# Optimization experiments

Hardware: AMD Instinct MI355X
Metric: run time of the kernel (lower is better)

## Reference

```python
import jax, jax.numpy as jnp
import numpy as np

N = 50000   # num_nodes
D = 128     # h_dim
R = 32      # num_rels * 2 (forward + inverse relations)
B = 8       # num_bases
E = 600000  # num_edges


def setup_inputs() -> dict:
    key = jax.random.key(0)
    ks = jax.random.split(key, 14)
    s = 1.0 / np.sqrt(D)
    return {
        "h_ids": jnp.arange(N, dtype=jnp.int32),
        "src": jax.random.randint(ks[0], (E,), 0, N),
        "dst": jax.random.randint(ks[1], (E,), 0, N),
        "etype": jax.random.randint(ks[2], (E,), 0, R),
        "norm": jax.random.uniform(ks[3], (E, 1), dtype=jnp.float32),
        "embedding": jax.random.normal(ks[4], (N, D), dtype=jnp.float32) * 0.05,
        "w_comp1": jax.random.normal(ks[5], (R, B), dtype=jnp.float32) * (1.0 / np.sqrt(B)),
        "bases1": jax.random.normal(ks[6], (B, D, D), dtype=jnp.float32) * s,
        "loop_w1": jax.random.normal(ks[7], (D, D), dtype=jnp.float32) * s,
        "bias1": jnp.zeros((D,), dtype=jnp.float32),
        "w_comp2": jax.random.normal(ks[8], (R, B), dtype=jnp.float32) * (1.0 / np.sqrt(B)),
        "bases2": jax.random.normal(ks[9], (B, D, D), dtype=jnp.float32) * s,
        "loop_w2": jax.random.normal(ks[10], (D, D), dtype=jnp.float32) * s,
        "bias2": jnp.zeros((D,), dtype=jnp.float32),
    }


def _rel_graph_conv(h, src, dst, etype, norm, w_comp, bases, loop_w, bias, act):
    # basis decomposition: W[r] = sum_b w_comp[r,b] * bases[b]
    W = jnp.einsum('rb,bio->rio', w_comp, bases)          # [R, D, D]
    # transform every node by every relation weight (dense GEMM)
    all_t = jnp.einsum('ni,rio->nro', h, W)               # [N, R, D]
    # per-edge gather of relation-specific transformed source features
    msg = all_t[src, etype] * norm                        # [E, D]
    # scatter-aggregate messages at destination nodes
    agg = jax.ops.segment_sum(msg, dst, num_segments=h.shape[0])  # [N, D]
    out = agg + h @ loop_w + bias                         # self-loop + bias
    return act(out) if act is not None else out


def reference(h_ids, src, dst, etype, norm, embedding,
              w_comp1, bases1, loop_w1, bias1,
              w_comp2, bases2, loop_w2, bias2):
    # EmbeddingLayer
    h = embedding[h_ids]                                  # [N, D]
    # hidden layer 0: relu activation (idx < num_hidden_layers-1)
    h = _rel_graph_conv(h, src, dst, etype, norm, w_comp1, bases1, loop_w1, bias1, jax.nn.relu)
    # hidden layer 1: no activation (last layer)
    h = _rel_graph_conv(h, src, dst, etype, norm, w_comp2, bases2, loop_w2, bias2, None)
    return h
```

## Files before the change

### kernel.cpp

```cpp
#include <hip/hip_runtime.h>

#define DD 128
#define NB 8
#define KTOT 1152

typedef unsigned int uint_t;
typedef __attribute__((ext_vector_type(8))) _Float16 half8v;
typedef __attribute__((ext_vector_type(2))) _Float16 half2v;
typedef __attribute__((ext_vector_type(4))) float f32x4;

static __device__ __forceinline__ void gld_lds16(const _Float16* g, _Float16* l)
{
  __builtin_amdgcn_global_load_lds(
      (const __attribute__((address_space(1))) void*)g,
      (__attribute__((address_space(3))) void*)l, 16, 0, 0);
}

static __device__ __forceinline__ half2v bc_h2(uint_t u)
{
  union { uint_t u; half2v h; } c; c.u = u; return c.h;
}

static __device__ __forceinline__ float fdot2(uint_t a, uint_t b, float acc)
{
#if __has_builtin(__builtin_amdgcn_fdot2)
  return __builtin_amdgcn_fdot2(bc_h2(a), bc_h2(b), acc, false);
#else
  half2v x = bc_h2(a), y = bc_h2(b);
  return acc + (float)x[0] * (float)y[0] + (float)x[1] * (float)y[1];
#endif
}

__global__ __launch_bounds__(256) void k_prep_w(
    const float* __restrict__ bases1, const float* __restrict__ loopw1,
    const float* __restrict__ bases2, const float* __restrict__ loopw2,
    _Float16* __restrict__ WcA)
{
  int i = blockIdx.x * 256 + threadIdx.x;
  if (i >= 2 * 36 * DD * 32) return;
  int layer = i / (36 * DD * 32);
  int rem   = i % (36 * DD * 32);
  int ks    = rem / (DD * 32);
  int rem2  = rem % (DD * 32);
  int feat  = rem2 / 32;
  int j     = rem2 % 32;
  int k     = ks * 32 + j;
  const float* basesL = layer ? bases2 : bases1;
  const float* loopwL = layer ? loopw2 : loopw1;
  float v;
  if (k < 1024) {
    int kk = k >> 3, b = k & 7;
    v = basesL[((size_t)b * DD + kk) * DD + feat];
  } else {
    v = loopwL[(size_t)(k - 1024) * DD + feat];
  }
  WcA[i] = (_Float16)v;
}

__global__ __launch_bounds__(256) void k_cast(
    const float* __restrict__ h, const int* __restrict__ ids,
    _Float16* __restrict__ hf, int N)
{
  int i = blockIdx.x * 256 + threadIdx.x;
  if (i >= N * (DD / 8)) return;
  int n  = i / (DD / 8);
  int k8 = (i % (DD / 8)) * 8;
  int row = ids ? ids[n] : n;
  const float* hp = h + (size_t)row * DD + k8;
  float4 v0 = *(const float4*)hp;
  float4 v1 = *(const float4*)(hp + 4);
  union { _Float16 e[8]; uint4 q; } p;
  p.e[0]=(_Float16)v0.x; p.e[1]=(_Float16)v0.y; p.e[2]=(_Float16)v0.z; p.e[3]=(_Float16)v0.w;
  p.e[4]=(_Float16)v1.x; p.e[5]=(_Float16)v1.y; p.e[6]=(_Float16)v1.z; p.e[7]=(_Float16)v1.w;
  *(uint4*)&hf[(size_t)n * DD + k8] = p.q;
}

__global__ __launch_bounds__(256) void k_zero(int* __restrict__ p, int n)
{
  int i = blockIdx.x * 256 + threadIdx.x;
  if (i < n) p[i] = 0;
}

__global__ __launch_bounds__(256) void k_hist(
    const int* __restrict__ dst, int* __restrict__ cnt, int E)
{
  int e = blockIdx.x * 256 + threadIdx.x;
  if (e < E) atomicAdd(&cnt[dst[e]], 1);
}

__global__ __launch_bounds__(256) void k_bsum(
    const int* __restrict__ cnt, int* __restrict__ bsum, int N)
{
  __shared__ int s[256];
  int i = blockIdx.x * 256 + threadIdx.x;
  s[threadIdx.x] = (i < N) ? ((cnt[i] + 1) & ~1) : 0;
  __syncthreads();
  for (int off = 128; off > 0; off >>= 1) {
    if (threadIdx.x < off) s[threadIdx.x] += s[threadIdx.x + off];
    __syncthreads();
  }
  if (threadIdx.x == 0) bsum[blockIdx.x] = s[0];
}

__global__ __launch_bounds__(256) void k_scanb(
    const int* __restrict__ bsum, int* __restrict__ boff, int nb)
{
  __shared__ int s[256];
  int t = threadIdx.x;
  int own = (t < nb) ? bsum[t] : 0;
  s[t] = own;
  __syncthreads();
  for (int off = 1; off < 256; off <<= 1) {
    int v = (t >= off) ? s[t - off] : 0;
    __syncthreads();
    s[t] += v;
    __syncthreads();
  }
  if (t < nb) boff[t] = s[t] - own;
}

__global__ __launch_bounds__(256) void k_scan3(
    const int* __restrict__ cnt, const int* __restrict__ boff,
    int* __restrict__ row_start, int N)
{
  __shared__ int s[256];
  int t = threadIdx.x;
  int i = blockIdx.x * 256 + t;
  int v = (i < N) ? ((cnt[i] + 1) & ~1) : 0;
  s[t] = v;
  __syncthreads();
  for (int off = 1; off < 256; off <<= 1) {
    int u = (t >= off) ? s[t - off] : 0;
    __syncthreads();
    s[t] += u;
    __syncthreads();
  }
  if (i < N) row_start[i] = boff[blockIdx.x] + s[t] - v;
}

__global__ __launch_bounds__(256) void k_place_payload(
    const int* __restrict__ dst, const int* __restrict__ src,
    const int* __restrict__ etype, const float* __restrict__ norm,
    const float* __restrict__ wcomp1, const float* __restrict__ wcomp2,
    const int* __restrict__ rowst, int* __restrict__ cursor,
    int* __restrict__ psrc, _Float16* __restrict__ c1, _Float16* __restrict__ c2,
    int E)
{
  int e = blockIdx.x * 256 + threadIdx.x;
  if (e >= E) return;
  int v = dst[e];
  int slot = rowst[v] + atomicAdd(&cursor[v], 1);
  psrc[slot] = src[e];
  int t = etype[e];
  float nm = norm[e];
  const float* w1 = wcomp1 + t * NB;
  const float* w2 = wcomp2 + t * NB;
  size_t base = (size_t)(slot >> 1) * 16 + (slot & 1);
  #pragma unroll
  for (int b = 0; b < NB; b++) c1[base + b * 2] = (_Float16)(w1[b] * nm);
  #pragma unroll
  for (int b = 0; b < NB; b++) c2[base + b * 2] = (_Float16)(w2[b] * nm);
}

__global__ __launch_bounds__(256) void k_agg(
    const int* __restrict__ rowst, const int* __restrict__ cnt,
    const int* __restrict__ psrc, const _Float16* __restrict__ cpair,
    const _Float16* __restrict__ hf,
    _Float16* __restrict__ agg, int N)
{
  int v = blockIdx.x * 4 + (threadIdx.x >> 6);
  if (v >= N) return;
  int lane = threadIdx.x & 63;
  const uint_t* hf32 = (const uint_t*)hf;
  const int beg = rowst[v];
  const int npairs = (cnt[v] + 1) >> 1;
  const uint_t* cp = (const uint_t*)cpair + (size_t)(beg >> 1) * 8;
  const int* ps = psrc + beg;

  float ax[NB] = {}, ay[NB] = {};
  int i = 0;
  for (; i + 2 <= npairs; i += 2) {
    int s0 = ps[2*i + 0], s1 = ps[2*i + 1];
    int s2 = ps[2*i + 2], s3 = ps[2*i + 3];
    uint_t u0 = hf32[(size_t)s0 * 64 + lane];
    uint_t u1 = hf32[(size_t)s1 * 64 + lane];
    uint_t u2 = hf32[(size_t)s2 * 64 + lane];
    uint_t u3 = hf32[(size_t)s3 * 64 + lane];
    uint_t lo01 = __builtin_amdgcn_perm(u0, u1, 0x01000504);
    uint_t hi01 = __builtin_amdgcn_perm(u0, u1, 0x03020706);
    uint_t lo23 = __builtin_amdgcn_perm(u2, u3, 0x01000504);
    uint_t hi23 = __builtin_amdgcn_perm(u2, u3, 0x03020706);
    #pragma unroll
    for (int b = 0; b < NB; b++) {
      uint_t ca = cp[(size_t)i * 8 + b];
      uint_t cb = cp[(size_t)(i + 1) * 8 + b];
      ax[b] = fdot2(ca, lo01, ax[b]);
      ay[b] = fdot2(ca, hi01, ay[b]);
      ax[b] = fdot2(cb, lo23, ax[b]);
      ay[b] = fdot2(cb, hi23, ay[b]);
    }
  }
  if (i < npairs) {
    int s0 = ps[2*i + 0], s1 = ps[2*i + 1];
    uint_t u0 = hf32[(size_t)s0 * 64 + lane];
    uint_t u1 = hf32[(size_t)s1 * 64 + lane];
    uint_t lo01 = __builtin_amdgcn_perm(u0, u1, 0x01000504);
    uint_t hi01 = __builtin_amdgcn_perm(u0, u1, 0x03020706);
    #pragma unroll
    for (int b = 0; b < NB; b++) {
      uint_t ca = cp[(size_t)i * 8 + b];
      ax[b] = fdot2(ca, lo01, ax[b]);
      ay[b] = fdot2(ca, hi01, ay[b]);
    }
  }

  union { _Float16 e[8]; uint4 q; } p0, p1;
  #pragma unroll
  for (int b = 0; b < NB; b++) { p0.e[b] = (_Float16)ax[b]; p1.e[b] = (_Float16)ay[b]; }
  uint4* dstp = (uint4*)&agg[(size_t)v * 1024 + lane * 16];
  dstp[0] = p0.q;
  dstp[1] = p1.q;
}

template <int LAYER>
__global__ __launch_bounds__(256) void k_mm(
    const _Float16* __restrict__ agg,
    const _Float16* __restrict__ hf,
    const _Float16* __restrict__ WcA,
    const float* __restrict__ bias,
    float* __restrict__ outf, _Float16* __restrict__ outh, int N)
{
  __shared__ _Float16 sB[2][4096];

  const int n0   = blockIdx.x * 64;
  const int wv   = threadIdx.x >> 6;
  const int lane = threadIdx.x & 63;
  const int l15  = lane & 15, l4 = lane >> 4;

  int nodeL = n0 + lane; if (nodeL >= N) nodeL = N - 1;

  f32x4 acc[2][4];
  #pragma unroll
  for (int a = 0; a < 2; a++)
    #pragma unroll
    for (int b = 0; b < 4; b++) acc[a][b] = (f32x4)0.f;

  const int fbase = wv * 32 + l15;
  const int koff  = l4 * 8;

  auto STAGE = [&](int buf, int t) {
    const _Float16 *g0, *g1;
    if (t < 16) {
      g0 = &agg[(size_t)nodeL * 1024 + (2 * t)     * 32 + wv * 8];
      g1 = &agg[(size_t)nodeL * 1024 + (2 * t + 1) * 32 + wv * 8];
    } else {
      g0 = &hf[(size_t)nodeL * DD + (2 * t - 32) * 32 + wv * 8];
      g1 = &hf[(size_t)nodeL * DD + (2 * t - 31) * 32 + wv * 8];
    }
    gld_lds16(g0, &sB[buf][ wv      * 512]);
    gld_lds16(g1, &sB[buf][(wv + 4) * 512]);
  };

  auto COMPUTE = [&](int buf, int t) {
    #pragma unroll
    for (int sub = 0; sub < 2; sub++) {
      const int ks = 2 * t + sub;
      half8v af[2], bfr[4];
      #pragma unroll
      for (int mf = 0; mf < 2; mf++)
        af[mf] = *(const half8v*)&WcA[((size_t)ks * DD + fbase + mf * 16) * 32 + koff];
      #pragma unroll
      for (int nf = 0; nf < 4; nf++)
        bfr[nf] = *(const half8v*)&sB[buf][(l4 + sub * 4) * 512 + (nf * 16 + l15) * 8];
      #pragma unroll
      for (int mf = 0; mf < 2; mf++)
        #pragma unroll
        for (int nf = 0; nf < 4; nf++)
          acc[mf][nf] = __builtin_amdgcn_mfma_f32_16x16x32_f16(af[mf], bfr[nf], acc[mf][nf], 0, 0, 0);
    }
  };

  STAGE(0, 0);
  __syncthreads();
  int cur = 0;
  for (int t = 0; t < 17; t++) {
    STAGE(cur ^ 1, t + 1);
    COMPUTE(cur, t);
    __syncthreads();
    cur ^= 1;
  }
  COMPUTE(cur, 17);

  #pragma unroll
  for (int mf = 0; mf < 2; mf++)
    #pragma unroll
    for (int nf = 0; nf < 4; nf++) {
      int n = n0 + nf * 16 + l15;
      if (n >= N) continue;
      int feat = wv * 32 + mf * 16 + l4 * 4;
      if (LAYER == 1) {
        union { _Float16 e[4]; uint2 q; } p;
        #pragma unroll
        for (int r = 0; r < 4; r++)
          p.e[r] = (_Float16)fmaxf(acc[mf][nf][r] + bias[feat + r], 0.f);
        *(uint2*)&outh[(size_t)n * DD + feat] = p.q;
      } else {
        float4 o;
        o.x = acc[mf][nf][0] + bias[feat + 0];
        o.y = acc[mf][nf][1] + bias[feat + 1];
        o.z = acc[mf][nf][2] + bias[feat + 2];
        o.w = acc[mf][nf][3] + bias[feat + 3];
        *(float4*)&outf[(size_t)n * DD + feat] = o;
      }
    }
}

extern "C" void kernel_launch(void* const* d_in, const int* in_sizes, int n_in,
                              void* d_out, int out_size, void* d_ws, size_t ws_size,
                              hipStream_t stream)
{
  const int*   h_ids     = (const int*)d_in[0];
  const int*   src       = (const int*)d_in[1];
  const int*   dst       = (const int*)d_in[2];
  const int*   etype     = (const int*)d_in[3];
  const float* norm      = (const float*)d_in[4];
  const float* embedding = (const float*)d_in[5];
  const float* w_comp1   = (const float*)d_in[6];
  const float* bases1    = (const float*)d_in[7];
  const float* loop_w1   = (const float*)d_in[8];
  const float* bias1     = (const float*)d_in[9];
  const float* w_comp2   = (const float*)d_in[10];
  const float* bases2    = (const float*)d_in[11];
  const float* loop_w2   = (const float*)d_in[12];
  const float* bias2     = (const float*)d_in[13];

  const int N = in_sizes[0];
  const int E = in_sizes[1];
  const int S = E + N;
  const int NBLK = (N + 255) / 256;

  char* base = (char*)d_ws;
  size_t off = 0;
  auto alloc = [&](size_t bytes) -> char* {
    char* p = base + off;
    off += (bytes + 255) & ~(size_t)255;
    return p;
  };
  _Float16* agg  = (_Float16*)alloc((size_t)N * 1024 * 2);
  _Float16* hfp  = (_Float16*)alloc((size_t)N * DD * 2);
  _Float16* h1h  = (_Float16*)alloc((size_t)N * DD * 2);
  _Float16* WcA  = (_Float16*)alloc((size_t)2 * 36 * DD * 32 * 2);
  int*      cnt    = (int*)   alloc((size_t)2 * N * 4);
  int*      cursor = cnt + N;
  int*      rowst  = (int*)   alloc((size_t)N * 4);
  int*      bsum   = (int*)   alloc(256 * 4);
  int*      boff   = (int*)   alloc(256 * 4);
  int*      psrc   = (int*)   alloc((size_t)S * 4);
  _Float16* c1     = (_Float16*)alloc((size_t)S * 8 * 2);
  _Float16* c2     = (_Float16*)alloc((size_t)S * 8 * 2);
  float*    out    = (float*)d_out;

  k_zero <<<(2 * N + 255) / 256, 256, 0, stream>>>(cnt, 2 * N);
  k_zero <<<(S + 255) / 256, 256, 0, stream>>>(psrc, S);
  k_zero <<<(S * 4 + 255) / 256, 256, 0, stream>>>((int*)c1, S * 4);
  k_zero <<<(S * 4 + 255) / 256, 256, 0, stream>>>((int*)c2, S * 4);
  k_hist <<<(E + 255) / 256, 256, 0, stream>>>(dst, cnt, E);
  k_bsum <<<NBLK, 256, 0, stream>>>(cnt, bsum, N);
  k_scanb<<<1, 256, 0, stream>>>(bsum, boff, NBLK);
  k_scan3<<<NBLK, 256, 0, stream>>>(cnt, boff, rowst, N);
  k_place_payload<<<(E + 255) / 256, 256, 0, stream>>>(
      dst, src, etype, norm, w_comp1, w_comp2, rowst, cursor, psrc, c1, c2, E);

  k_prep_w<<<(2 * 36 * DD * 32 + 255) / 256, 256, 0, stream>>>(bases1, loop_w1, bases2, loop_w2, WcA);

  dim3 gmm((N + 63) / 64);
  int gagg = (N + 3) / 4;

  k_cast<<<(N * (DD / 8) + 255) / 256, 256, 0, stream>>>(embedding, h_ids, hfp, N);
  k_agg<<<gagg, 256, 0, stream>>>(rowst, cnt, psrc, c1, hfp, agg, N);
  k_mm<1><<<gmm, 256, 0, stream>>>(agg, hfp, WcA, bias1, nullptr, h1h, N);

  k_agg<<<gagg, 256, 0, stream>>>(rowst, cnt, psrc, c2, h1h, agg, N);
  k_mm<2><<<gmm, 256, 0, stream>>>(agg, h1h, WcA + (size_t)36 * DD * 32, bias2, out, nullptr, N);
}
```

Baseline: 290.6 us.

## Split edge placement into permutation pass and coalesced pair-payload writer

Edge placement now scatters only the edge index into a permutation array. A second kernel walks destination-sorted slots in pairs and writes psrc and the interleaved fp16 coefficient payloads with vector stores. This removes the three full zeroing passes over psrc, c1 and c2 (padding slots are marked -1 in perm) and turns scattered 2-byte stores into coalesced 16-byte stores. The cost is one extra kernel launch and gathered reads of src, etype and norm through perm.

```diff
diff --git a/kernel.cpp b/kernel.cpp
--- a/kernel.cpp
+++ b/kernel.cpp
@@ -81,6 +81,12 @@
   if (i < n) p[i] = 0;
 }
 
+__global__ __launch_bounds__(256) void k_fill(int* __restrict__ p, int val, int n)
+{
+  int i = blockIdx.x * 256 + threadIdx.x;
+  if (i < n) p[i] = val;
+}
+
 __global__ __launch_bounds__(256) void k_hist(
     const int* __restrict__ dst, int* __restrict__ cnt, int E)
 {
@@ -138,28 +144,52 @@
   if (i < N) row_start[i] = boff[blockIdx.x] + s[t] - v;
 }
 
-__global__ __launch_bounds__(256) void k_place_payload(
-    const int* __restrict__ dst, const int* __restrict__ src,
+__global__ __launch_bounds__(256) void k_place(
+    const int* __restrict__ dst, const int* __restrict__ row_start,
+    int* __restrict__ cursor, int* __restrict__ perm, int E)
+{
+  int e = blockIdx.x * 256 + threadIdx.x;
+  if (e < E) {
+    int v = dst[e];
+    int slot = row_start[v] + atomicAdd(&cursor[v], 1);
+    perm[slot] = e;
+  }
+}
+
+__global__ __launch_bounds__(256) void k_payload_pair(
+    const int* __restrict__ perm, const int* __restrict__ src,
     const int* __restrict__ etype, const float* __restrict__ norm,
     const float* __restrict__ wcomp1, const float* __restrict__ wcomp2,
-    const int* __restrict__ rowst, int* __restrict__ cursor,
     int* __restrict__ psrc, _Float16* __restrict__ c1, _Float16* __restrict__ c2,
-    int E)
-{
-  int e = blockIdx.x * 256 + threadIdx.x;
-  if (e >= E) return;
-  int v = dst[e];
-  int slot = rowst[v] + atomicAdd(&cursor[v], 1);
-  psrc[slot] = src[e];
-  int t = etype[e];
-  float nm = norm[e];
-  const float* w1 = wcomp1 + t * NB;
-  const float* w2 = wcomp2 + t * NB;
-  size_t base = (size_t)(slot >> 1) * 16 + (slot & 1);
+    int npair)
+{
+  int i = blockIdx.x * 256 + threadIdx.x;
+  if (i >= npair) return;
+  int e0 = perm[2 * i], e1 = perm[2 * i + 1];
+
+  int s0 = 0, s1 = 0;
+  float n0 = 0.f, n1 = 0.f;
+  const float *w10 = wcomp1, *w20 = wcomp2, *w11 = wcomp1, *w21 = wcomp2;
+  if (e0 >= 0) { s0 = src[e0]; n0 = norm[e0]; int t = etype[e0]; w10 = wcomp1 + t * NB; w20 = wcomp2 + t * NB; }
+  if (e1 >= 0) { s1 = src[e1]; n1 = norm[e1]; int t = etype[e1]; w11 = wcomp1 + t * NB; w21 = wcomp2 + t * NB; }
+
+  *(int2*)&psrc[2 * i] = make_int2(s0, s1);
+
+  union { _Float16 h[16]; uint4 q[2]; } p;
   #pragma unroll
-  for (int b = 0; b < NB; b++) c1[base + b * 2] = (_Float16)(w1[b] * nm);
+  for (int b = 0; b < NB; b++) {
+    p.h[b * 2]     = (_Float16)(w10[b] * n0);
+    p.h[b * 2 + 1] = (_Float16)(w11[b] * n1);
+  }
+  *(uint4*)&c1[(size_t)i * 16]     = p.q[0];
+  *(uint4*)&c1[(size_t)i * 16 + 8] = p.q[1];
   #pragma unroll
-  for (int b = 0; b < NB; b++) c2[base + b * 2] = (_Float16)(w2[b] * nm);
+  for (int b = 0; b < NB; b++) {
+    p.h[b * 2]     = (_Float16)(w20[b] * n0);
+    p.h[b * 2 + 1] = (_Float16)(w21[b] * n1);
+  }
+  *(uint4*)&c2[(size_t)i * 16]     = p.q[0];
+  *(uint4*)&c2[(size_t)i * 16 + 8] = p.q[1];
 }
 
 __global__ __launch_bounds__(256) void k_agg(
@@ -336,7 +366,8 @@
 
   const int N = in_sizes[0];
   const int E = in_sizes[1];
-  const int S = E + N;
+  const int S = (E + N) & ~1;
+  const int NPAIR = S >> 1;
   const int NBLK = (N + 255) / 256;
 
   char* base = (char*)d_ws;
@@ -355,21 +386,21 @@
   int*      rowst  = (int*)   alloc((size_t)N * 4);
   int*      bsum   = (int*)   alloc(256 * 4);
   int*      boff   = (int*)   alloc(256 * 4);
+  int*      perm   = (int*)   alloc((size_t)S * 4);
   int*      psrc   = (int*)   alloc((size_t)S * 4);
   _Float16* c1     = (_Float16*)alloc((size_t)S * 8 * 2);
   _Float16* c2     = (_Float16*)alloc((size_t)S * 8 * 2);
   float*    out    = (float*)d_out;
 
   k_zero <<<(2 * N + 255) / 256, 256, 0, stream>>>(cnt, 2 * N);
-  k_zero <<<(S + 255) / 256, 256, 0, stream>>>(psrc, S);
-  k_zero <<<(S * 4 + 255) / 256, 256, 0, stream>>>((int*)c1, S * 4);
-  k_zero <<<(S * 4 + 255) / 256, 256, 0, stream>>>((int*)c2, S * 4);
+  k_fill <<<(S + 255) / 256, 256, 0, stream>>>(perm, -1, S);
   k_hist <<<(E + 255) / 256, 256, 0, stream>>>(dst, cnt, E);
   k_bsum <<<NBLK, 256, 0, stream>>>(cnt, bsum, N);
   k_scanb<<<1, 256, 0, stream>>>(bsum, boff, NBLK);
   k_scan3<<<NBLK, 256, 0, stream>>>(cnt, boff, rowst, N);
-  k_place_payload<<<(E + 255) / 256, 256, 0, stream>>>(
-      dst, src, etype, norm, w_comp1, w_comp2, rowst, cursor, psrc, c1, c2, E);
+  k_place<<<(E + 255) / 256, 256, 0, stream>>>(dst, rowst, cursor, perm, E);
+  k_payload_pair<<<(NPAIR + 255) / 256, 256, 0, stream>>>(
+      perm, src, etype, norm, w_comp1, w_comp2, psrc, c1, c2, NPAIR);
 
   k_prep_w<<<(2 * 36 * DD * 32 + 255) / 256, 256, 0, stream>>>(bases1, loop_w1, bases2, loop_w2, WcA);
 
```

New measurement: 276.2 us. 5.0% less time.
